# Kernel optimization log

Hardware: AMD Instinct MI355X
Metric: run time of the kernel (lower is better)

## Reference

```python
import jax, jax.numpy as jnp
import numpy as np

LABELS = (1, 2, 3)  # from init_kwargs
EPS = float(np.finfo(np.float32).eps)
SHAPE = (512, 512, 512)


def setup_inputs() -> dict:
    key = jax.random.key(0)
    k1, k2 = jax.random.split(key)
    # label maps with values in {0,1,2,3}, stored as float32 (equality-compared)
    vol1 = jax.random.randint(k1, SHAPE, 0, 4).astype(jnp.float32)
    vol2 = jax.random.randint(k2, SHAPE, 0, 4).astype(jnp.float32)
    return {"vol1": vol1, "vol2": vol2}


def reference(vol1, vol2):
    # Per-label Dice: dice_l = 2*|A_l & B_l| / (|A_l| + |B_l| + eps)
    dices = []
    for lab in LABELS:  # fixed tiny label set -> loop is fine
        labv = jnp.asarray(lab, dtype=vol1.dtype)
        m1 = vol1 == labv
        m2 = vol2 == labv
        top = 2.0 * jnp.sum(m1 & m2).astype(jnp.float32)
        bottom = jnp.sum(m1).astype(jnp.float32) + jnp.sum(m2).astype(jnp.float32)
        dices.append(top / (bottom + EPS))
    dicem = jnp.stack(dices)
    return 1.0 - jnp.mean(dicem)
```

## Files before the change

### kernel.cpp

```cpp
#include <hip/hip_runtime.h>
#include <stdint.h>


#define NCNT 9
#define NBLK 2048
#define TPB  256

typedef unsigned int v4u __attribute__((ext_vector_type(4)));
typedef __attribute__((address_space(3))) uint8_t lds8_t;
typedef __attribute__((address_space(1))) const uint8_t glb8_t;

#define F1 0x3F800000u
#define F2 0x40000000u
#define F3 0x40400000u

__device__ __forceinline__ void count4u(v4u x, v4u y, unsigned int* c) {
#pragma unroll
    for (int comp = 0; comp < 4; ++comp) {
        const unsigned v = x[comp];
        const unsigned w = y[comp];
        bool a1 = (v == F1), a2 = (v == F2), a3 = (v == F3);
        bool b1 = (w == F1), b2 = (w == F2), b3 = (w == F3);
        c[0] += a1; c[1] += a2; c[2] += a3;
        c[3] += b1; c[4] += b2; c[5] += b3;
        c[6] += a1 & b1; c[7] += a2 & b2; c[8] += a3 & b3;
    }
}

__global__ __launch_bounds__(TPB, 8) void dice_count(const uint8_t* __restrict__ a,
                                                     const uint8_t* __restrict__ b,
                                                     unsigned int* __restrict__ partials,
                                                     long long n_bytes) {
    __shared__ uint8_t smem[16384];

    unsigned int c[NCNT];
#pragma unroll
    for (int k = 0; k < NCNT; ++k) c[k] = 0u;

    const int w = threadIdx.x >> 6;
    const int l = threadIdx.x & 63;

    const long long block_bytes = 8192;
    const long long gstride = (long long)gridDim.x * block_bytes;
    const int iters = (int)(n_bytes / gstride);

    lds8_t* la = (lds8_t*)&smem[w * 2048];
    lds8_t* lb = (lds8_t*)&smem[8192 + w * 2048];
    const v4u* ra = (const v4u*)&smem[w * 2048 + l * 16];
    const v4u* rb = (const v4u*)&smem[8192 + w * 2048 + l * 16];

    for (int j = 0; j < iters; ++j) {
        const long long base = (long long)j * gstride
                             + (long long)blockIdx.x * block_bytes
                             + (long long)w * 2048 + (long long)l * 16;
        __builtin_amdgcn_global_load_lds((glb8_t*)(a + base),        la,        16, 0, 0);
        __builtin_amdgcn_global_load_lds((glb8_t*)(a + base + 1024), la + 1024, 16, 0, 0);
        __builtin_amdgcn_global_load_lds((glb8_t*)(b + base),        lb,        16, 0, 0);
        __builtin_amdgcn_global_load_lds((glb8_t*)(b + base + 1024), lb + 1024, 16, 0, 0);
        __builtin_amdgcn_sched_barrier(0);
        __builtin_amdgcn_s_waitcnt(0xF70);
        __builtin_amdgcn_sched_barrier(0);
        v4u xa0 = ra[0], xa1 = ra[64];
        v4u yb0 = rb[0], yb1 = rb[64];
        count4u(xa0, yb0, c);
        count4u(xa1, yb1, c);
    }

    {
        const long long done = (long long)iters * gstride;
        const unsigned int* au = (const unsigned int*)a;
        const unsigned int* bu = (const unsigned int*)b;
        const long long n_elem = n_bytes >> 2;
        for (long long e = (done >> 2) + blockIdx.x * TPB + threadIdx.x;
             e < n_elem; e += (long long)gridDim.x * TPB) {
            const unsigned v = au[e];
            const unsigned ww = bu[e];
            bool a1 = (v == F1), a2 = (v == F2), a3 = (v == F3);
            bool b1 = (ww == F1), b2 = (ww == F2), b3 = (ww == F3);
            c[0] += a1; c[1] += a2; c[2] += a3;
            c[3] += b1; c[4] += b2; c[5] += b3;
            c[6] += a1 & b1; c[7] += a2 & b2; c[8] += a3 & b3;
        }
    }

#pragma unroll
    for (int k = 0; k < NCNT; ++k) {
#pragma unroll
        for (int off = 32; off > 0; off >>= 1)
            c[k] += __shfl_down(c[k], off, 64);
    }

    __syncthreads();
    unsigned int* s = (unsigned int*)smem;
    if (l == 0) {
#pragma unroll
        for (int k = 0; k < NCNT; ++k) s[w * NCNT + k] = c[k];
    }
    __syncthreads();
    if (threadIdx.x == 0) {
#pragma unroll
        for (int k = 0; k < NCNT; ++k) {
            partials[blockIdx.x * NCNT + k] =
                s[0 * NCNT + k] + s[1 * NCNT + k] + s[2 * NCNT + k] + s[3 * NCNT + k];
        }
    }
}

__global__ __launch_bounds__(TPB) void dice_finalize(const unsigned int* __restrict__ partials,
                                                     float* __restrict__ out, int nblk) {
    unsigned int c[NCNT];
#pragma unroll
    for (int k = 0; k < NCNT; ++k) c[k] = 0u;
    for (int bidx = threadIdx.x; bidx < nblk; bidx += TPB) {
#pragma unroll
        for (int k = 0; k < NCNT; ++k) c[k] += partials[bidx * NCNT + k];
    }
#pragma unroll
    for (int k = 0; k < NCNT; ++k) {
#pragma unroll
        for (int off = 32; off > 0; off >>= 1)
            c[k] += __shfl_down(c[k], off, 64);
    }
    __shared__ unsigned int s[4][NCNT];
    const int w = threadIdx.x >> 6;
    const int l = threadIdx.x & 63;
    if (l == 0) {
#pragma unroll
        for (int k = 0; k < NCNT; ++k) s[w][k] = c[k];
    }
    __syncthreads();
    if (threadIdx.x == 0) {
        const double eps = 1.1920928955078125e-07;
        double acc = 0.0;
#pragma unroll
        for (int lab = 0; lab < 3; ++lab) {
            double c1 = (double)(s[0][lab] + s[1][lab] + s[2][lab] + s[3][lab]);
            double c2 = (double)(s[0][3 + lab] + s[1][3 + lab] + s[2][3 + lab] + s[3][3 + lab]);
            double in = (double)(s[0][6 + lab] + s[1][6 + lab] + s[2][6 + lab] + s[3][6 + lab]);
            acc += (2.0 * in) / (c1 + c2 + eps);
        }
        out[0] = (float)(1.0 - acc / 3.0);
    }
}

extern "C" void kernel_launch(void* const* d_in, const int* in_sizes, int n_in,
                              void* d_out, int out_size, void* d_ws, size_t ws_size,
                              hipStream_t stream) {
    const uint8_t* v1 = (const uint8_t*)d_in[0];
    const uint8_t* v2 = (const uint8_t*)d_in[1];
    float* out = (float*)d_out;
    unsigned int* partials = (unsigned int*)d_ws;

    const long long n_bytes = (long long)in_sizes[0] * 4;

    dice_count<<<NBLK, TPB, 0, stream>>>(v1, v2, partials, n_bytes);
    dice_finalize<<<1, TPB, 0, stream>>>(partials, out, NBLK);
}
```

Baseline: 969.7 us.

## Double-buffer LDS loads to overlap the next fetch with counting

Replaces the load-wait-compute loop with a two-stage software pipeline. Each wave prefetches the next slab into an alternate LDS buffer while counting the current one, using a partial vmcnt wait. The per-iteration chunk is halved so each thread loads one 16-byte vector per input per stage, which doubles the iteration count. This hides global load latency at the cost of more loop overhead and smaller in-flight transfers per wave.

Result: no change. 985.6 us (+1.6%).

```diff
diff --git a/kernel.cpp b/kernel.cpp
--- a/kernel.cpp
+++ b/kernel.cpp
@@ -40,30 +40,40 @@
     const int w = threadIdx.x >> 6;
     const int l = threadIdx.x & 63;
 
-    const long long block_bytes = 8192;
+    const long long block_bytes = 4096;
     const long long gstride = (long long)gridDim.x * block_bytes;
     const int iters = (int)(n_bytes / gstride);
 
-    lds8_t* la = (lds8_t*)&smem[w * 2048];
-    lds8_t* lb = (lds8_t*)&smem[8192 + w * 2048];
-    const v4u* ra = (const v4u*)&smem[w * 2048 + l * 16];
-    const v4u* rb = (const v4u*)&smem[8192 + w * 2048 + l * 16];
+    lds8_t* la[2] = { (lds8_t*)&smem[w * 4096],
+                      (lds8_t*)&smem[w * 4096 + 1024] };
+    lds8_t* lb[2] = { (lds8_t*)&smem[w * 4096 + 2048],
+                      (lds8_t*)&smem[w * 4096 + 3072] };
+    const v4u* ra[2] = { (const v4u*)&smem[w * 4096 + l * 16],
+                         (const v4u*)&smem[w * 4096 + 1024 + l * 16] };
+    const v4u* rb[2] = { (const v4u*)&smem[w * 4096 + 2048 + l * 16],
+                         (const v4u*)&smem[w * 4096 + 3072 + l * 16] };
 
-    for (int j = 0; j < iters; ++j) {
-        const long long base = (long long)j * gstride
-                             + (long long)blockIdx.x * block_bytes
-                             + (long long)w * 2048 + (long long)l * 16;
-        __builtin_amdgcn_global_load_lds((glb8_t*)(a + base),        la,        16, 0, 0);
-        __builtin_amdgcn_global_load_lds((glb8_t*)(a + base + 1024), la + 1024, 16, 0, 0);
-        __builtin_amdgcn_global_load_lds((glb8_t*)(b + base),        lb,        16, 0, 0);
-        __builtin_amdgcn_global_load_lds((glb8_t*)(b + base + 1024), lb + 1024, 16, 0, 0);
-        __builtin_amdgcn_sched_barrier(0);
+    const long long wave_off = (long long)blockIdx.x * block_bytes
+                             + (long long)w * 1024 + (long long)l * 16;
+
+    if (iters > 0) {
+        __builtin_amdgcn_global_load_lds((glb8_t*)(a + wave_off), la[0], 16, 0, 0);
+        __builtin_amdgcn_global_load_lds((glb8_t*)(b + wave_off), lb[0], 16, 0, 0);
+
+        for (int j = 0; j + 1 < iters; ++j) {
+            const int cur = j & 1, nxt = cur ^ 1;
+            const long long nbase = wave_off + (long long)(j + 1) * gstride;
+            __builtin_amdgcn_global_load_lds((glb8_t*)(a + nbase), la[nxt], 16, 0, 0);
+            __builtin_amdgcn_global_load_lds((glb8_t*)(b + nbase), lb[nxt], 16, 0, 0);
+            __builtin_amdgcn_sched_barrier(0);
+            __builtin_amdgcn_s_waitcnt(0xF72);
+            __builtin_amdgcn_sched_barrier(0);
+            count4u(ra[cur][0], rb[cur][0], c);
+            __builtin_amdgcn_sched_barrier(0);
+        }
         __builtin_amdgcn_s_waitcnt(0xF70);
         __builtin_amdgcn_sched_barrier(0);
-        v4u xa0 = ra[0], xa1 = ra[64];
-        v4u yb0 = rb[0], yb1 = rb[64];
-        count4u(xa0, yb0, c);
-        count4u(xa1, yb1, c);
+        count4u(ra[(iters - 1) & 1][0], rb[(iters - 1) & 1][0], c);
     }
 
     {
```
